# Kernel optimization log

Hardware: AMD Instinct MI355X
Metric: run time of the kernel (lower is better)

The kernel has to match this reference:

```python
import jax, jax.numpy as jnp
import numpy as np

B, T, F, H, O = 128, 512, 512, 1024, 1


def setup_inputs() -> dict:
    key = jax.random.key(0)
    ks = jax.random.split(key, 11)
    s_ih1 = 1.0 / np.sqrt(H)
    return {
        "x": jax.random.normal(ks[0], (B, T, F), dtype=jnp.float32),
        # LSTMCell params, torch layout: weight_ih [4H, in], weight_hh [4H, H]
        "W_ih1": jax.random.uniform(ks[1], (4 * H, F), jnp.float32, -s_ih1, s_ih1),
        "W_hh1": jax.random.uniform(ks[2], (4 * H, H), jnp.float32, -s_ih1, s_ih1),
        "b_ih1": jax.random.uniform(ks[3], (4 * H,), jnp.float32, -s_ih1, s_ih1),
        "b_hh1": jax.random.uniform(ks[4], (4 * H,), jnp.float32, -s_ih1, s_ih1),
        "W_ih2": jax.random.uniform(ks[5], (4 * H, H), jnp.float32, -s_ih1, s_ih1),
        "W_hh2": jax.random.uniform(ks[6], (4 * H, H), jnp.float32, -s_ih1, s_ih1),
        "b_ih2": jax.random.uniform(ks[7], (4 * H,), jnp.float32, -s_ih1, s_ih1),
        "b_hh2": jax.random.uniform(ks[8], (4 * H,), jnp.float32, -s_ih1, s_ih1),
        "W_lin": jax.random.uniform(ks[9], (O, H), jnp.float32, -s_ih1, s_ih1),
        "b_lin": jax.random.uniform(ks[10], (O,), jnp.float32, -s_ih1, s_ih1),
    }


def _lstm_cell(x_t, h, c, W_ih, W_hh, b_ih, b_hh):
    # gates: [B, 4H]; torch gate order i, f, g, o
    gates = x_t @ W_ih.T + b_ih + h @ W_hh.T + b_hh
    i, f, g, o = jnp.split(gates, 4, axis=-1)
    i, f, o = jax.nn.sigmoid(i), jax.nn.sigmoid(f), jax.nn.sigmoid(o)
    g = jnp.tanh(g)
    c_new = f * c + i * g
    h_new = o * jnp.tanh(c_new)
    return h_new, c_new


def reference(x, W_ih1, W_hh1, b_ih1, b_hh1, W_ih2, W_hh2, b_ih2, b_hh2, W_lin, b_lin):
    B_, dtype = x.shape[0], x.dtype
    zeros = jnp.zeros((B_, H), dtype=dtype)
    init = (zeros, zeros, zeros, zeros)  # h1, c1, h2, c2

    def step(carry, x_t):
        h1, c1, h2, c2 = carry
        h1, c1 = _lstm_cell(x_t, h1, c1, W_ih1, W_hh1, b_ih1, b_hh1)
        h2, c2 = _lstm_cell(h1, h2, c2, W_ih2, W_hh2, b_ih2, b_hh2)
        return (h1, c1, h2, c2), None

    (h1, c1, h2, c2), _ = jax.lax.scan(step, init, jnp.swapaxes(x, 0, 1))
    # linear applied to the last timestep's h2 only (loop overwrites output)
    return h2 @ W_lin.T + b_lin
```

## Files before the change

kernel.cpp:

```cpp
#include <hip/hip_runtime.h>

#define Bb  128
#define Tt  512
#define Ff  512
#define Hh  1024
#define BH  (Bb*Hh)
#define WGS 512
#define NBLK 256
#define NPH 515
#define PBH (128*4096)

#define OFF_H1   0u
#define OFF_H2   524288u
#define OFF_H2F  1048576u
#define OFF_BAR  1572864u
#define OFF_PB   1576960u
#define OFF_PBX  5771264u
#define OFF_XB   9965568u
#define WS_NEED  77074432u

typedef __attribute__((ext_vector_type(8))) short short8;
typedef __attribute__((ext_vector_type(4))) float f32x4;
typedef __attribute__((ext_vector_type(16))) float f32x16;

__device__ __forceinline__ short f2bf(float f){
  union { float fv; unsigned u; } v; v.fv = f;
  unsigned r = v.u + 0x7fffu + ((v.u >> 16) & 1u);
  return (short)(r >> 16);
}
__device__ __forceinline__ float sigm(float x){ return 1.f/(1.f+__expf(-x)); }

__device__ __forceinline__ f32x16 mfma32(short8 a, short8 b, f32x16 c){
  return __builtin_amdgcn_mfma_f32_32x32x16_bf16(a, b, c, 0, 0, 0);
}

__device__ __forceinline__ short8 scld8(const short* p){
  short8 d;
  asm volatile("global_load_dwordx4 %0, %1, off sc0 sc1" : "=v"(d) : "v"(p) : "memory");
  return d;
}
__device__ __forceinline__ f32x4 scldf4(const float* p){
  f32x4 d;
  asm volatile("global_load_dwordx4 %0, %1, off sc0 sc1" : "=v"(d) : "v"(p) : "memory");
  return d;
}
__device__ __forceinline__ void sstf4(float* p, f32x4 v){
  asm volatile("global_store_dwordx4 %0, %1, off sc0 sc1" :: "v"(p), "v"(v) : "memory");
}
__device__ __forceinline__ void ssth(short* p, short v){
  asm volatile("global_store_short %0, %1, off sc0 sc1"
               :: "v"(p), "v"((unsigned)(unsigned short)v) : "memory");
}
__device__ __forceinline__ void drain_vm(){
  asm volatile("s_waitcnt vmcnt(0)" ::: "memory");
  __builtin_amdgcn_sched_barrier(0);
}

__global__ void __launch_bounds__(WGS) conv_x(const float* __restrict__ xf,
                                              short* __restrict__ xb){
  const size_t i = ((size_t)blockIdx.x * WGS + threadIdx.x) * 8;
  float4 u0 = *(const float4*)(xf + i);
  float4 u1 = *(const float4*)(xf + i + 4);
  short8 v;
  v[0]=f2bf(u0.x); v[1]=f2bf(u0.y); v[2]=f2bf(u0.z); v[3]=f2bf(u0.w);
  v[4]=f2bf(u1.x); v[5]=f2bf(u1.y); v[6]=f2bf(u1.z); v[7]=f2bf(u1.w);
  *(short8*)(xb + i) = v;
}

__global__ void __launch_bounds__(WGS, 2) lstm4(
    const short* __restrict__ xb,
    const float* __restrict__ Wih1, const float* __restrict__ Whh1,
    const float* __restrict__ bih1, const float* __restrict__ bhh1,
    const float* __restrict__ Wih2, const float* __restrict__ Whh2,
    const float* __restrict__ bih2, const float* __restrict__ bhh2,
    short* __restrict__ h1, short* __restrict__ h2,
    float* __restrict__ PB, float* __restrict__ PBX,
    float* __restrict__ h2f32, unsigned* __restrict__ bar)
{
  extern __shared__ char lds[];
  float* F  = (float*)lds;
  float* Lb = (float*)(lds + 131072);

  const int bid = blockIdx.x, tid = threadIdx.x;
  const int grp = bid >> 6;
  const int cu  = bid & 63;
  const int c0h = cu << 4;
  const int lane = tid & 63, wv = tid >> 6;
  const int tc = lane & 31, hi = lane >> 5;
  const int slot = bid & 7;

  const int cth = wv & 1;
  const int kh  = (wv >> 1) & 1;
  const int rh  = wv >> 2;
  const int xrt = wv >> 1;

  if (tid < 64){
    const int hc = tid >> 2, g = tid & 3;
    float v = 0.f;
    if (grp == 0) v = bih1[(g<<10) + c0h + hc] + bhh1[(g<<10) + c0h + hc];
    if (grp == 2) v = bih2[(g<<10) + c0h + hc] + bhh2[(g<<10) + c0h + hc];
    Lb[tid] = v;
  }

  const float* Wsrc = (grp==0) ? Whh1 : (grp==1) ? Wih2 : (grp==2) ? Whh2 : Wih1;
  const int Kdim = (grp==3) ? Ff : Hh;
  const int kb0  = (grp==3) ? 0 : kh*512;
  const int wrow = (tc&3)*Hh + c0h + cth*8 + (tc>>2);
  short8 bfr[32];
  #pragma unroll
  for (int f = 0; f < 32; ++f){
    const float* s = Wsrc + (size_t)wrow*Kdim + kb0 + f*16 + hi*8;
    float4 u0 = *(const float4*)(s);
    float4 u1 = *(const float4*)(s + 4);
    short8 v;
    v[0]=f2bf(u0.x); v[1]=f2bf(u0.y); v[2]=f2bf(u0.z); v[3]=f2bf(u0.w);
    v[4]=f2bf(u1.x); v[5]=f2bf(u1.y); v[6]=f2bf(u1.z); v[7]=f2bf(u1.w);
    bfr[f] = v;
  }
  __syncthreads();

  float cst[4] = {0.f, 0.f, 0.f, 0.f};
  const int swz = (lane & 31) << 4;

  for (int p = 0; p < NPH; ++p){
    const bool act = (grp==0) ? (p>=1 && p<=512)
                   : (grp==1) ? (p>=2 && p<=513)
                   : (grp==2) ? (p>=3 && p<=514)
                   :            (p < 512);
    const short* sh = (grp==2) ? (h2 + (p&1)*BH) : (h1 + (p&1)*BH);

    f32x4 pre[4] = {{0,0,0,0},{0,0,0,0},{0,0,0,0},{0,0,0,0}};
    if (act && (grp == 0 || grp == 2)){
      const float* src = (grp == 0) ? (PBX + (size_t)((p+1)&1)*PBH)
                                    : (PB  + (size_t)((p+1)&1)*PBH);
      #pragma unroll
      for (int s4 = 0; s4 < 4; ++s4){
        const int id = (s4<<9) + tid;
        pre[s4] = scldf4(src + (size_t)(id>>4)*4096 + ((c0h + (id&15))<<2));
      }
    }

    f32x16 a0, a1;
    #pragma unroll
    for (int i = 0; i < 16; ++i){ a0[i] = 0.f; a1[i] = 0.f; }

    #pragma unroll
    for (int r = 0; r < 2; ++r){
      if (act){
        if (grp != 3){
          #pragma unroll
          for (int buf = 0; buf < 2; ++buf){
            const int kq = 2*buf + r;
            short8 t[8];
            #pragma unroll
            for (int i = 0; i < 8; ++i){
              const int u = (i<<9) + tid;
              t[i] = scld8(sh + (size_t)(u>>5)*Hh + kq*256 + (u&31)*8);
            }
            drain_vm();
            #pragma unroll
            for (int i = 0; i < 8; ++i){
              const int u = (i<<9) + tid;
              *(short8*)(lds + buf*65536 + (((u<<4)) ^ ((((u>>5)&31))<<4))) = t[i];
            }
          }
        } else {
          short8 t[8];
          #pragma unroll
          for (int i = 0; i < 8; ++i){
            const int u = (i<<9) + tid;
            t[i] = *(const short8*)(xb + ((size_t)(u>>5)*Tt + p)*Ff + r*256 + (u&31)*8);
          }
          #pragma unroll
          for (int i = 0; i < 8; ++i){
            const int u = (i<<9) + tid;
            *(short8*)(lds + r*65536 + (((u<<4)) ^ ((((u>>5)&31))<<4))) = t[i];
          }
        }
      }
      __syncthreads();
      if (act){
        if (grp != 3){
          const int row0 = rh*64 + (lane & 31);
          const char* b0 = lds + kh*65536 + row0*512;
          const char* b1 = b0 + 32*512;
          #pragma unroll
          for (int ci = 0; ci < 16; ++ci){
            const int ko = (((ci<<5) | (hi<<4)) ^ swz);
            short8 A0 = *(const short8*)(b0 + ko);
            short8 A1 = *(const short8*)(b1 + ko);
            a0 = mfma32(A0, bfr[r*16+ci], a0);
            a1 = mfma32(A1, bfr[r*16+ci], a1);
          }
        } else {
          const int row0 = xrt*32 + (lane & 31);
          const char* b0 = lds + r*65536 + row0*512;
          #pragma unroll
          for (int ci = 0; ci < 16; ++ci){
            const int ko = (((ci<<5) | (hi<<4)) ^ swz);
            short8 A0 = *(const short8*)(b0 + ko);
            a0 = mfma32(A0, bfr[r*16+ci], a0);
          }
        }
      }
      __syncthreads();
    }

    if (act){
      const int colf = (cth<<5) + tc;
      if (grp != 3){
        #pragma unroll
        for (int rg = 0; rg < 16; ++rg){
          const int rl = (rg&3) + ((rg>>2)<<3) + (hi<<2);
          F[(kh*128 + rh*64 + rl)*68 + colf]      = a0[rg];
          F[(kh*128 + rh*64 + 32 + rl)*68 + colf] = a1[rg];
        }
      } else {
        #pragma unroll
        for (int rg = 0; rg < 16; ++rg){
          const int rl = (rg&3) + ((rg>>2)<<3) + (hi<<2);
          F[(xrt*32 + rl)*68 + colf] = a0[rg];
        }
      }
    }
    __syncthreads();

    if (act){
      #pragma unroll
      for (int s = 0; s < 4; ++s){
        const int id  = (s<<9) + tid;
        const int row = id >> 4, hc = id & 15;
        const int gc4 = (c0h + hc) << 2;
        f32x4 q = *(f32x4*)&F[row*68 + (hc<<2)];
        if (grp != 3) q += *(f32x4*)&F[(128+row)*68 + (hc<<2)];
        if (grp == 0){
          f32x4 bb = *(f32x4*)&Lb[hc<<2];
          float gi=q[0]+pre[s][0]+bb[0], gf=q[1]+pre[s][1]+bb[1];
          float gg=q[2]+pre[s][2]+bb[2], go=q[3]+pre[s][3]+bb[3];
          float iv=sigm(gi), fv=sigm(gf), gv=tanhf(gg), ov=sigm(go);
          cst[s] = fv*cst[s] + iv*gv;
          ssth(h1 + ((p+1)&1)*BH + row*Hh + c0h + hc, f2bf(ov*tanhf(cst[s])));
        } else if (grp == 1){
          sstf4(PB + (size_t)(p&1)*PBH + row*4096 + gc4, q);
        } else if (grp == 2){
          f32x4 bb = *(f32x4*)&Lb[hc<<2];
          float gi=q[0]+pre[s][0]+bb[0], gf=q[1]+pre[s][1]+bb[1];
          float gg=q[2]+pre[s][2]+bb[2], go=q[3]+pre[s][3]+bb[3];
          float iv=sigm(gi), fv=sigm(gf), gv=tanhf(gg), ov=sigm(go);
          cst[s] = fv*cst[s] + iv*gv;
          float hv = ov*tanhf(cst[s]);
          ssth(h2 + ((p+1)&1)*BH + row*Hh + c0h + hc, f2bf(hv));
          if (p == 514) h2f32[row*Hh + c0h + hc] = hv;
        } else {
          sstf4(PBX + (size_t)(p&1)*PBH + row*4096 + gc4, q);
        }
      }
    }

    __syncthreads();
    if (tid == 0){
      unsigned prev = __hip_atomic_fetch_add(bar + (slot<<6), 1u,
                        __ATOMIC_RELAXED, __HIP_MEMORY_SCOPE_AGENT);
      if (prev == 32u*(p+1) - 1u)
        __hip_atomic_fetch_add(bar + 768, 1u,
                        __ATOMIC_RELAXED, __HIP_MEMORY_SCOPE_AGENT);
      while (__hip_atomic_load(bar + 768,
                        __ATOMIC_RELAXED, __HIP_MEMORY_SCOPE_AGENT) < 8u*(p+1))
        __builtin_amdgcn_s_sleep(1);
    }
    __syncthreads();
  }
}

__global__ void final_linear(const float* __restrict__ h2, const float* __restrict__ Wl,
                             const float* __restrict__ bl, float* __restrict__ out){
  __shared__ float red[256];
  const int b = blockIdx.x, t = threadIdx.x;
  float s = 0.f;
  for (int k = t; k < Hh; k += 256) s += h2[(size_t)b*Hh + k] * Wl[k];
  red[t] = s; __syncthreads();
  for (int off = 128; off > 0; off >>= 1){ if (t < off) red[t] += red[t+off]; __syncthreads(); }
  if (t == 0) out[b] = red[0] + bl[0];
}

extern "C" void kernel_launch(void* const* d_in, const int* in_sizes, int n_in,
                              void* d_out, int out_size, void* d_ws, size_t ws_size,
                              hipStream_t stream) {
  (void)in_sizes; (void)n_in; (void)out_size;
  const float* x    = (const float*)d_in[0];
  const float* Wih1 = (const float*)d_in[1];
  const float* Whh1 = (const float*)d_in[2];
  const float* bih1 = (const float*)d_in[3];
  const float* bhh1 = (const float*)d_in[4];
  const float* Wih2 = (const float*)d_in[5];
  const float* Whh2 = (const float*)d_in[6];
  const float* bih2 = (const float*)d_in[7];
  const float* bhh2 = (const float*)d_in[8];
  const float* Wlin = (const float*)d_in[9];
  const float* blin = (const float*)d_in[10];
  float* out = (float*)d_out;

  if (ws_size < WS_NEED) return;
  char* ws = (char*)d_ws;
  short*    h1b   = (short*)(ws + OFF_H1);
  short*    h2b   = (short*)(ws + OFF_H2);
  float*    h2f32 = (float*)(ws + OFF_H2F);
  unsigned* bar   = (unsigned*)(ws + OFF_BAR);
  float*    PB    = (float*)(ws + OFF_PB);
  float*    PBX   = (float*)(ws + OFF_PBX);
  short*    xb    = (short*)(ws + OFF_XB);

  hipMemsetAsync(d_ws, 0, OFF_PB, stream);
  conv_x<<<dim3(8192), dim3(WGS), 0, stream>>>(x, xb);
  hipFuncSetAttribute(reinterpret_cast<const void*>(lstm4),
                      hipFuncAttributeMaxDynamicSharedMemorySize, 131584);
  lstm4<<<dim3(NBLK), dim3(WGS), 131584, stream>>>(
      xb, Wih1, Whh1, bih1, bhh1, Wih2, Whh2, bih2, bhh2,
      h1b, h2b, PB, PBX, h2f32, bar);
  final_linear<<<dim3(Bb), dim3(256), 0, stream>>>(h2f32, Wlin, blin, out);
}
```

Before: 9.456 ms.

## Retile LSTM blocks as 64 rows × 32 hidden columns with single-pass K staging

Each block now owns a 64-batch-row by 32-hidden-column tile instead of all 128 rows by 16 columns. It stages its whole K range for its rows into LDS in one pass, replacing the previous two-round staging with four syncs per phase. Each wave handles one K-half and one column group, issuing two MFMA chains over 32 steps, and the F reduction buffer is reshaped to match. The aim is to halve the hidden-state bytes each block loads and to cut barriers per timestep. In exchange, launch bounds drop to one block per SM and register and LDS pressure rise.

```diff
diff --git a/kernel.cpp b/kernel.cpp
--- a/kernel.cpp
+++ b/kernel.cpp
@@ -8,7 +8,7 @@
 #define WGS 512
 #define NBLK 256
 #define NPH 515
-#define PBH (128*4096)
+#define PBH (Bb*4096)
 
 #define OFF_H1   0u
 #define OFF_H2   524288u
@@ -67,7 +67,7 @@
   *(short8*)(xb + i) = v;
 }
 
-__global__ void __launch_bounds__(WGS, 2) lstm4(
+__global__ void __launch_bounds__(WGS, 1) lstm4(
     const short* __restrict__ xb,
     const float* __restrict__ Wih1, const float* __restrict__ Whh1,
     const float* __restrict__ bih1, const float* __restrict__ bhh1,
@@ -83,144 +83,134 @@
 
   const int bid = blockIdx.x, tid = threadIdx.x;
   const int grp = bid >> 6;
-  const int cu  = bid & 63;
-  const int c0h = cu << 4;
+  const int sub = bid & 63;
+  const int rbase = (sub >> 5) << 6;
+  const int c0  = (sub & 31) << 5;
   const int lane = tid & 63, wv = tid >> 6;
   const int tc = lane & 31, hi = lane >> 5;
+  const int kh = wv & 1, cth = wv >> 1;
+  const int t256 = (cth << 6) + lane;
   const int slot = bid & 7;
 
-  const int cth = wv & 1;
-  const int kh  = (wv >> 1) & 1;
-  const int rh  = wv >> 2;
-  const int xrt = wv >> 1;
-
-  if (tid < 64){
+  if (tid < 128){
     const int hc = tid >> 2, g = tid & 3;
     float v = 0.f;
-    if (grp == 0) v = bih1[(g<<10) + c0h + hc] + bhh1[(g<<10) + c0h + hc];
-    if (grp == 2) v = bih2[(g<<10) + c0h + hc] + bhh2[(g<<10) + c0h + hc];
+    if (grp == 0) v = bih1[(g<<10)+c0+hc] + bhh1[(g<<10)+c0+hc];
+    if (grp == 2) v = bih2[(g<<10)+c0+hc] + bhh2[(g<<10)+c0+hc];
     Lb[tid] = v;
   }
 
-  const float* Wsrc = (grp==0) ? Whh1 : (grp==1) ? Wih2 : (grp==2) ? Whh2 : Wih1;
-  const int Kdim = (grp==3) ? Ff : Hh;
-  const int kb0  = (grp==3) ? 0 : kh*512;
-  const int wrow = (tc&3)*Hh + c0h + cth*8 + (tc>>2);
+  const float* Wsrc = (grp==0)?Whh1:(grp==1)?Wih2:(grp==2)?Whh2:Wih1;
+  const int wrow = (tc&3)*Hh + c0 + (cth<<3) + (tc>>2);
   short8 bfr[32];
-  #pragma unroll
-  for (int f = 0; f < 32; ++f){
-    const float* s = Wsrc + (size_t)wrow*Kdim + kb0 + f*16 + hi*8;
-    float4 u0 = *(const float4*)(s);
-    float4 u1 = *(const float4*)(s + 4);
-    short8 v;
-    v[0]=f2bf(u0.x); v[1]=f2bf(u0.y); v[2]=f2bf(u0.z); v[3]=f2bf(u0.w);
-    v[4]=f2bf(u1.x); v[5]=f2bf(u1.y); v[6]=f2bf(u1.z); v[7]=f2bf(u1.w);
-    bfr[f] = v;
+  if (grp != 3){
+    const float* wb = Wsrc + (size_t)wrow*Hh + (kh<<9) + (hi<<3);
+    #pragma unroll
+    for (int f = 0; f < 32; ++f){
+      float4 u0 = *(const float4*)(wb + (f<<4));
+      float4 u1 = *(const float4*)(wb + (f<<4) + 4);
+      short8 v;
+      v[0]=f2bf(u0.x); v[1]=f2bf(u0.y); v[2]=f2bf(u0.z); v[3]=f2bf(u0.w);
+      v[4]=f2bf(u1.x); v[5]=f2bf(u1.y); v[6]=f2bf(u1.z); v[7]=f2bf(u1.w);
+      bfr[f] = v;
+    }
+  } else {
+    const float* wb = Wsrc + (size_t)wrow*Ff + (kh<<8) + (hi<<3);
+    #pragma unroll
+    for (int f = 0; f < 16; ++f){
+      float4 u0 = *(const float4*)(wb + (f<<4));
+      float4 u1 = *(const float4*)(wb + (f<<4) + 4);
+      short8 v;
+      v[0]=f2bf(u0.x); v[1]=f2bf(u0.y); v[2]=f2bf(u0.z); v[3]=f2bf(u0.w);
+      v[4]=f2bf(u1.x); v[5]=f2bf(u1.y); v[6]=f2bf(u1.z); v[7]=f2bf(u1.w);
+      bfr[f] = v;
+    }
   }
   __syncthreads();
 
-  float cst[4] = {0.f, 0.f, 0.f, 0.f};
-  const int swz = (lane & 31) << 4;
+  float cst[4] = {0.f,0.f,0.f,0.f};
 
   for (int p = 0; p < NPH; ++p){
     const bool act = (grp==0) ? (p>=1 && p<=512)
                    : (grp==1) ? (p>=2 && p<=513)
                    : (grp==2) ? (p>=3 && p<=514)
                    :            (p < 512);
-    const short* sh = (grp==2) ? (h2 + (p&1)*BH) : (h1 + (p&1)*BH);
+    const short* sh = ((grp==2) ? h2 : h1) + (p&1)*BH;
 
     f32x4 pre[4] = {{0,0,0,0},{0,0,0,0},{0,0,0,0},{0,0,0,0}};
-    if (act && (grp == 0 || grp == 2)){
-      const float* src = (grp == 0) ? (PBX + (size_t)((p+1)&1)*PBH)
-                                    : (PB  + (size_t)((p+1)&1)*PBH);
-      #pragma unroll
-      for (int s4 = 0; s4 < 4; ++s4){
-        const int id = (s4<<9) + tid;
-        pre[s4] = scldf4(src + (size_t)(id>>4)*4096 + ((c0h + (id&15))<<2));
-      }
-    }
+
+    if (act){
+      short8 t[16];
+      if (grp == 0 || grp == 2){
+        const float* src = ((grp==0)?PBX:PB) + (size_t)((p+1)&1)*PBH;
+        #pragma unroll
+        for (int s4 = 0; s4 < 4; ++s4){
+          const int id = (s4<<9)+tid;
+          pre[s4] = scldf4(src + (size_t)(rbase + (id>>5))*4096 + ((c0 + (id&31))<<2));
+        }
+      }
+      if (grp != 3){
+        #pragma unroll
+        for (int i = 0; i < 16; ++i){
+          const int u = (i<<8)+t256;
+          t[i] = scld8(sh + (size_t)(rbase + (u>>6))*Hh + (kh<<9) + ((u&63)<<3));
+        }
+        drain_vm();
+        #pragma unroll
+        for (int i = 0; i < 16; ++i){
+          const int u = (i<<8)+t256, row = u>>6;
+          *(short8*)(lds + (kh<<16) + (row<<10) + ((((u&63)<<4)) ^ (row<<4))) = t[i];
+        }
+      } else {
+        #pragma unroll
+        for (int i = 0; i < 8; ++i){
+          const int u = (i<<8)+t256;
+          t[i] = *(const short8*)(xb + ((size_t)(rbase + (u>>5))*Tt + p)*Ff + (kh<<8) + ((u&31)<<3));
+        }
+        drain_vm();
+        #pragma unroll
+        for (int i = 0; i < 8; ++i){
+          const int u = (i<<8)+t256, row = u>>5;
+          *(short8*)(lds + (kh<<15) + (row<<9) + ((((u&31)<<4)) ^ ((row&31)<<4))) = t[i];
+        }
+      }
+    }
+    __syncthreads();
 
     f32x16 a0, a1;
     #pragma unroll
-    for (int i = 0; i < 16; ++i){ a0[i] = 0.f; a1[i] = 0.f; }
-
-    #pragma unroll
-    for (int r = 0; r < 2; ++r){
-      if (act){
-        if (grp != 3){
-          #pragma unroll
-          for (int buf = 0; buf < 2; ++buf){
-            const int kq = 2*buf + r;
-            short8 t[8];
-            #pragma unroll
-            for (int i = 0; i < 8; ++i){
-              const int u = (i<<9) + tid;
-              t[i] = scld8(sh + (size_t)(u>>5)*Hh + kq*256 + (u&31)*8);
-            }
-            drain_vm();
-            #pragma unroll
-            for (int i = 0; i < 8; ++i){
-              const int u = (i<<9) + tid;
-              *(short8*)(lds + buf*65536 + (((u<<4)) ^ ((((u>>5)&31))<<4))) = t[i];
-            }
-          }
-        } else {
-          short8 t[8];
-          #pragma unroll
-          for (int i = 0; i < 8; ++i){
-            const int u = (i<<9) + tid;
-            t[i] = *(const short8*)(xb + ((size_t)(u>>5)*Tt + p)*Ff + r*256 + (u&31)*8);
-          }
-          #pragma unroll
-          for (int i = 0; i < 8; ++i){
-            const int u = (i<<9) + tid;
-            *(short8*)(lds + r*65536 + (((u<<4)) ^ ((((u>>5)&31))<<4))) = t[i];
-          }
-        }
-      }
-      __syncthreads();
-      if (act){
-        if (grp != 3){
-          const int row0 = rh*64 + (lane & 31);
-          const char* b0 = lds + kh*65536 + row0*512;
-          const char* b1 = b0 + 32*512;
-          #pragma unroll
-          for (int ci = 0; ci < 16; ++ci){
-            const int ko = (((ci<<5) | (hi<<4)) ^ swz);
-            short8 A0 = *(const short8*)(b0 + ko);
-            short8 A1 = *(const short8*)(b1 + ko);
-            a0 = mfma32(A0, bfr[r*16+ci], a0);
-            a1 = mfma32(A1, bfr[r*16+ci], a1);
-          }
-        } else {
-          const int row0 = xrt*32 + (lane & 31);
-          const char* b0 = lds + r*65536 + row0*512;
-          #pragma unroll
-          for (int ci = 0; ci < 16; ++ci){
-            const int ko = (((ci<<5) | (hi<<4)) ^ swz);
-            short8 A0 = *(const short8*)(b0 + ko);
-            a0 = mfma32(A0, bfr[r*16+ci], a0);
-          }
-        }
-      }
-      __syncthreads();
-    }
+    for (int i = 0; i < 16; ++i){ a0[i]=0.f; a1[i]=0.f; }
+
+    if (act){
+      if (grp != 3){
+        const int r0 = tc, r1 = 32+tc;
+        const char* base = lds + (kh<<16);
+        #pragma unroll
+        for (int ci = 0; ci < 32; ++ci){
+          const int ko = (ci<<5) | (hi<<4);
+          a0 = mfma32(*(const short8*)(base + (r0<<10) + (ko ^ (r0<<4))), bfr[ci], a0);
+          a1 = mfma32(*(const short8*)(base + (r1<<10) + (ko ^ (r1<<4))), bfr[ci], a1);
+        }
+      } else {
+        const int r0 = tc, r1 = 32+tc;
+        const char* base = lds + (kh<<15);
+        #pragma unroll
+        for (int ci = 0; ci < 16; ++ci){
+          const int ko = (ci<<5) | (hi<<4);
+          a0 = mfma32(*(const short8*)(base + (r0<<9) + (ko ^ ((r0&31)<<4))), bfr[ci], a0);
+          a1 = mfma32(*(const short8*)(base + (r1<<9) + (ko ^ ((r1&31)<<4))), bfr[ci], a1);
+        }
+      }
+    }
+    __syncthreads();
 
     if (act){
       const int colf = (cth<<5) + tc;
-      if (grp != 3){
-        #pragma unroll
-        for (int rg = 0; rg < 16; ++rg){
-          const int rl = (rg&3) + ((rg>>2)<<3) + (hi<<2);
-          F[(kh*128 + rh*64 + rl)*68 + colf]      = a0[rg];
-          F[(kh*128 + rh*64 + 32 + rl)*68 + colf] = a1[rg];
-        }
-      } else {
-        #pragma unroll
-        for (int rg = 0; rg < 16; ++rg){
-          const int rl = (rg&3) + ((rg>>2)<<3) + (hi<<2);
-          F[(xrt*32 + rl)*68 + colf] = a0[rg];
-        }
+      #pragma unroll
+      for (int rg = 0; rg < 16; ++rg){
+        const int rl = (rg&3) + ((rg>>2)<<3) + (hi<<2);
+        F[((kh<<6) + rl)*132 + colf]      = a0[rg];
+        F[((kh<<6) + 32 + rl)*132 + colf] = a1[rg];
       }
     }
     __syncthreads();
@@ -228,31 +218,27 @@
     if (act){
       #pragma unroll
       for (int s = 0; s < 4; ++s){
-        const int id  = (s<<9) + tid;
-        const int row = id >> 4, hc = id & 15;
-        const int gc4 = (c0h + hc) << 2;
-        f32x4 q = *(f32x4*)&F[row*68 + (hc<<2)];
-        if (grp != 3) q += *(f32x4*)&F[(128+row)*68 + (hc<<2)];
-        if (grp == 0){
-          f32x4 bb = *(f32x4*)&Lb[hc<<2];
-          float gi=q[0]+pre[s][0]+bb[0], gf=q[1]+pre[s][1]+bb[1];
-          float gg=q[2]+pre[s][2]+bb[2], go=q[3]+pre[s][3]+bb[3];
-          float iv=sigm(gi), fv=sigm(gf), gv=tanhf(gg), ov=sigm(go);
-          cst[s] = fv*cst[s] + iv*gv;
-          ssth(h1 + ((p+1)&1)*BH + row*Hh + c0h + hc, f2bf(ov*tanhf(cst[s])));
-        } else if (grp == 1){
-          sstf4(PB + (size_t)(p&1)*PBH + row*4096 + gc4, q);
-        } else if (grp == 2){
+        const int id = (s<<9)+tid, row = id>>5, hc = id&31;
+        f32x4 q = *(f32x4*)&F[row*132 + (hc<<2)];
+        q += *(f32x4*)&F[(64+row)*132 + (hc<<2)];
+        const int grow = rbase + row, gcol = c0 + hc;
+        if (grp == 0 || grp == 2){
           f32x4 bb = *(f32x4*)&Lb[hc<<2];
           float gi=q[0]+pre[s][0]+bb[0], gf=q[1]+pre[s][1]+bb[1];
           float gg=q[2]+pre[s][2]+bb[2], go=q[3]+pre[s][3]+bb[3];
           float iv=sigm(gi), fv=sigm(gf), gv=tanhf(gg), ov=sigm(go);
           cst[s] = fv*cst[s] + iv*gv;
           float hv = ov*tanhf(cst[s]);
-          ssth(h2 + ((p+1)&1)*BH + row*Hh + c0h + hc, f2bf(hv));
-          if (p == 514) h2f32[row*Hh + c0h + hc] = hv;
+          if (grp == 0){
+            ssth(h1 + ((p+1)&1)*BH + (size_t)grow*Hh + gcol, f2bf(hv));
+          } else {
+            ssth(h2 + ((p+1)&1)*BH + (size_t)grow*Hh + gcol, f2bf(hv));
+            if (p == 514) h2f32[(size_t)grow*Hh + gcol] = hv;
+          }
+        } else if (grp == 1){
+          sstf4(PB + (size_t)(p&1)*PBH + (size_t)grow*4096 + (gcol<<2), q);
         } else {
-          sstf4(PBX + (size_t)(p&1)*PBH + row*4096 + gc4, q);
+          sstf4(PBX + (size_t)(p&1)*PBH + (size_t)grow*4096 + (gcol<<2), q);
         }
       }
     }
```

Measured after the change: 14.89 ms. 1.57x slower.
